# Performance work log

Measured on AMD Instinct MI355X. Metric: run time of the kernel, lower is better.

The kernel has to match this reference:

```python
import jax, jax.numpy as jnp
import numpy as np

MODEL_DIM = 1024
NUM_HEADS = 16
HEAD_DIM = MODEL_DIM // NUM_HEADS  # 64
MAX_SEQ = 1024
MAX_REL = 8


def setup_inputs() -> dict:
    key = jax.random.key(0)
    ks = jax.random.split(key, 5)
    B, S = 4, 1024
    x = jax.random.normal(ks[0], (B, S, MODEL_DIM), jnp.float32)
    W_in = jax.random.normal(ks[1], (MODEL_DIM, MODEL_DIM), jnp.float32) * 0.02
    W_out = jax.random.normal(ks[2], (MODEL_DIM, MODEL_DIM), jnp.float32) * 0.02
    # learned synthesized attention scores [1, H, max_seq, max_seq]
    attn_scores = jax.random.normal(ks[3], (1, NUM_HEADS, MAX_SEQ, MAX_SEQ), jnp.float32) * 0.05
    # relative-position VALUE embedding table [2*max_rel+1, head_dim]
    rel_values = jax.random.normal(ks[4], (2 * MAX_REL + 1, HEAD_DIM), jnp.float32) * 0.02
    return {"x": x, "W_in": W_in, "W_out": W_out,
            "attn_scores": attn_scores, "rel_values": rel_values}


def reference(x, W_in, W_out, attn_scores, rel_values):
    B, S, D = x.shape
    H, hd = NUM_HEADS, HEAD_DIM
    # in-projection (no bias), split heads: [B, H, S, hd]
    value = (x @ W_in.T).reshape(B, S, H, hd).transpose(0, 2, 1, 3)
    # learned (random-synthesizer) scores, sliced to seq len, broadcast over batch
    scores = attn_scores[:, :, :S, :S]              # [1, H, S, S]
    probs = jax.nn.softmax(scores, axis=-1)          # [1, H, S, S]
    probs = jnp.broadcast_to(probs, (B, H, S, S))
    # attention output: probs @ V
    out = jnp.einsum('bhsj,bhjd->bhsd', probs, value)  # [B, H, S, hd]
    # relative-position value contribution
    r = jnp.arange(S)
    dist = r[None, :] - r[:, None]                   # [S, S]
    idx = jnp.clip(dist, -MAX_REL, MAX_REL) + MAX_REL
    rel_emb = rel_values[idx]                        # [S, S, hd]
    out = out + jnp.einsum('bhsj,sjd->bhsd', probs, rel_emb)
    # join heads and out-project
    out = out.transpose(0, 2, 1, 3).reshape(B, S, H * hd)
    return out @ W_out.T                             # [B, S, D]
```

## Files before the change

kernel.cpp:

```cpp
#include <hip/hip_runtime.h>

typedef unsigned short ushort_t;
typedef __attribute__((ext_vector_type(4))) short short4_t;
typedef __attribute__((ext_vector_type(8))) short short8;
typedef __attribute__((ext_vector_type(4))) float floatx4;
typedef __attribute__((ext_vector_type(8))) __bf16 bf16x8;

__device__ __forceinline__ ushort_t f2b(float f) {
  union { float f; unsigned int i; } t; t.f = f;
  unsigned int u = t.i;
  return (ushort_t)((u + 0x7fffu + ((u >> 16) & 1u)) >> 16);
}

__device__ __forceinline__ floatx4 mfma16(short8 a, short8 b, floatx4 c) {
  return __builtin_amdgcn_mfma_f32_16x16x32_bf16(
      __builtin_bit_cast(bf16x8, a), __builtin_bit_cast(bf16x8, b), c, 0, 0, 0);
}

__device__ __forceinline__ void gload16(const void* g, void* l) {
  __builtin_amdgcn_global_load_lds(
      (const __attribute__((address_space(1))) void*)g,
      (__attribute__((address_space(3))) void*)l, 16, 0, 0);
}

__global__ __launch_bounds__(256) void k_f2b_all(
    const float* __restrict__ x, const float* __restrict__ Wi,
    const float* __restrict__ Wo, ushort_t* __restrict__ xb,
    ushort_t* __restrict__ Wib, ushort_t* __restrict__ Wob)
{
  const float* in; ushort_t* out; int i;
  if (blockIdx.x < 2048)      { in = x;  out = xb;  i = (blockIdx.x * 256 + threadIdx.x) * 8; }
  else if (blockIdx.x < 2560) { in = Wi; out = Wib; i = ((blockIdx.x - 2048) * 256 + threadIdx.x) * 8; }
  else                        { in = Wo; out = Wob; i = ((blockIdx.x - 2560) * 256 + threadIdx.x) * 8; }
  float4 a = *reinterpret_cast<const float4*>(in + i);
  float4 b = *reinterpret_cast<const float4*>(in + i + 4);
  short8 o;
  o[0] = (short)f2b(a.x); o[1] = (short)f2b(a.y);
  o[2] = (short)f2b(a.z); o[3] = (short)f2b(a.w);
  o[4] = (short)f2b(b.x); o[5] = (short)f2b(b.y);
  o[6] = (short)f2b(b.z); o[7] = (short)f2b(b.w);
  *reinterpret_cast<short8*>(out + i) = o;
}

#define STG(kt, buf, SLOTSZ)                                                \
  {                                                                         \
    const int k0 = (kt) << 6;                                               \
    _Pragma("unroll")                                                       \
    for (int cc = 0; cc < 2; ++cc) {                                        \
      int c = threadIdx.x + (cc << 9);                                      \
      int r = c >> 3, cb = c & 7;                                           \
      int sc = k0 + ((cb ^ (r & 7)) << 3);                                  \
      gload16(A0 + (size_t)r * 1024 + sc, (char*)sA + (buf) * SLOTSZ + c * 16); \
      gload16(B0 + (size_t)r * 1024 + sc, (char*)sB + (buf) * SLOTSZ + c * 16); \
    }                                                                       \
  }

#define KSTEP_COMPUTE(bA, bB)                                               \
  _Pragma("unroll")                                                         \
  for (int kk = 0; kk < 2; ++kk) {                                          \
    const int cs = (kk << 2) + lk;                                          \
    short8 af[4], bf[2];                                                    \
    _Pragma("unroll")                                                       \
    for (int i = 0; i < 4; ++i) {                                           \
      int ra = (wm << 6) + (i << 4) + l15;                                  \
      af[i] = *reinterpret_cast<const short8*>(                             \
          (bA) + ra * 128 + ((cs ^ (ra & 7)) << 4));                        \
    }                                                                       \
    _Pragma("unroll")                                                       \
    for (int j = 0; j < 2; ++j) {                                           \
      int rb = (wn << 5) + (j << 4) + l15;                                  \
      bf[j] = *reinterpret_cast<const short8*>(                             \
          (bB) + rb * 128 + ((cs ^ (rb & 7)) << 4));                        \
    }                                                                       \
    __builtin_amdgcn_s_setprio(1);                                          \
    _Pragma("unroll")                                                       \
    for (int i = 0; i < 4; ++i)                                             \
      _Pragma("unroll")                                                     \
      for (int j = 0; j < 2; ++j)                                           \
        acc[i][j] = mfma16(af[i], bf[j], acc[i][j]);                        \
    __builtin_amdgcn_s_setprio(0);                                          \
  }

__device__ __forceinline__ void gemm128_loop4(
    const ushort_t* __restrict__ A0, const ushort_t* __restrict__ B0,
    ushort_t* sA, ushort_t* sB, floatx4 (&acc)[4][2])
{
  const int lane = threadIdx.x & 63, wave = threadIdx.x >> 6;
  const int wm = wave & 1, wn = wave >> 1;
  const int l15 = lane & 15, lk = lane >> 4;

  STG(0, 0, 16384);
  STG(1, 1, 16384);
  for (int kt = 0; kt < 16; ++kt) {
    if (kt < 14) {
      STG(kt + 2, (kt + 2) & 3, 16384);
      asm volatile("s_waitcnt vmcnt(8)" ::: "memory");
    } else if (kt == 14) {
      asm volatile("s_waitcnt vmcnt(4)" ::: "memory");
    } else {
      asm volatile("s_waitcnt vmcnt(0)" ::: "memory");
    }
    __builtin_amdgcn_s_barrier();
    const char* bA = (const char*)sA + (kt & 3) * 16384;
    const char* bB = (const char*)sB + (kt & 3) * 16384;
    KSTEP_COMPUTE(bA, bB);
  }
}

__device__ __forceinline__ void gemm128_loop2(
    const ushort_t* __restrict__ A0, const ushort_t* __restrict__ B0,
    ushort_t* sA, ushort_t* sB, floatx4 (&acc)[4][2])
{
  const int lane = threadIdx.x & 63, wave = threadIdx.x >> 6;
  const int wm = wave & 1, wn = wave >> 1;
  const int l15 = lane & 15, lk = lane >> 4;

  STG(0, 0, 16384);
  for (int kt = 0; kt < 16; ++kt) {
    __syncthreads();
    if (kt < 15) STG(kt + 1, (kt + 1) & 1, 16384);
    const char* bA = (const char*)sA + (kt & 1) * 16384;
    const char* bB = (const char*)sB + (kt & 1) * 16384;
    KSTEP_COMPUTE(bA, bB);
  }
}

__device__ __forceinline__ int xcd_swz(int bid) {
  return ((bid & 7) << 5) | (bid >> 3);
}

__global__ __launch_bounds__(512) void k_fused_sm_xw(
    const float* __restrict__ S, const float* __restrict__ relv,
    ushort_t* __restrict__ P, float* __restrict__ R,
    const ushort_t* __restrict__ W, const ushort_t* __restrict__ X,
    ushort_t* __restrict__ Yt)
{
  __shared__ __align__(16) char smem[65536];

  if (blockIdx.x < 256) {
    ushort_t* sA = (ushort_t*)smem;
    ushort_t* sB = (ushort_t*)(smem + 32768);
    const int lg = xcd_swz(blockIdx.x);
    const int m0 = (lg & 7) << 7, n0 = (lg >> 3) << 7;
    const ushort_t* A0 = W + (size_t)m0 * 1024;
    const ushort_t* B0 = X + (size_t)n0 * 1024;
    floatx4 acc[4][2] = {};
    gemm128_loop2(A0, B0, sA, sB, acc);

    const int lane = threadIdx.x & 63, wave = threadIdx.x >> 6;
    const int wm = wave & 1, wn = wave >> 1;
    const int l15 = lane & 15, lk = lane >> 4;
#pragma unroll
    for (int i = 0; i < 4; ++i)
#pragma unroll
      for (int j = 0; j < 2; ++j)
#pragma unroll
        for (int rr = 0; rr < 4; ++rr) {
          int wrow = m0 + (wm << 6) + (i << 4) + (lk << 2) + rr;
          int col  = n0 + (wn << 5) + (j << 4) + l15;
          int h = wrow >> 6, d = wrow & 63;
          int b = col >> 10, s = col & 1023;
          Yt[(((size_t)((h << 2) + b) << 6) + d) * 1024 + s] = f2b(acc[i][j][rr]);
        }
    return;
  }

  float (*mid)[16] = (float (*)[16])smem;
  const int wave = threadIdx.x >> 6, lane = threadIdx.x & 63;
  const int row = (blockIdx.x - 256) * 8 + wave;
  const int s = row & 1023;
  const float* src = S + (size_t)row * 1024;

  float v[4][4];
#pragma unroll
  for (int c = 0; c < 4; ++c) {
    float4 raw = *reinterpret_cast<const float4*>(src + c * 256 + lane * 4);
    v[c][0] = raw.x; v[c][1] = raw.y; v[c][2] = raw.z; v[c][3] = raw.w;
  }
  float m = -1e30f;
#pragma unroll
  for (int c = 0; c < 4; ++c)
#pragma unroll
    for (int e = 0; e < 4; ++e) m = fmaxf(m, v[c][e]);
#pragma unroll
  for (int d = 32; d; d >>= 1) m = fmaxf(m, __shfl_xor(m, d));

  float p[4][4];
  float tot = 0.f, sA = 0.f, sB = 0.f;
#pragma unroll
  for (int c = 0; c < 4; ++c) {
#pragma unroll
    for (int e = 0; e < 4; ++e) {
      int j = c * 256 + lane * 4 + e;
      float pe = __expf(v[c][e] - m);
      p[c][e] = pe;
      tot += pe;
      sA += (j <= s - 8) ? pe : 0.f;
      sB += (j >= s + 8) ? pe : 0.f;
    }
  }
#pragma unroll
  for (int d = 32; d; d >>= 1) {
    tot += __shfl_xor(tot, d);
    sA  += __shfl_xor(sA, d);
    sB  += __shfl_xor(sB, d);
  }
  const float inv = 1.0f / tot;

  if (lane < 16) mid[wave][lane] = 0.f;
  __syncthreads();
#pragma unroll
  for (int c = 0; c < 4; ++c) {
#pragma unroll
    for (int e = 0; e < 4; ++e) {
      int j = c * 256 + lane * 4 + e;
      int tt = j - (s - 7);
      if (tt >= 0 && tt < 15) mid[wave][tt] = p[c][e];
    }
  }
  __syncthreads();

  float acc = sA * relv[lane] + sB * relv[16 * 64 + lane];
#pragma unroll
  for (int tt = 0; tt < 15; ++tt)
    acc += mid[wave][tt] * relv[(1 + tt) * 64 + lane];
  R[(size_t)row * 64 + lane] = acc * inv;

#pragma unroll
  for (int c = 0; c < 4; ++c) {
    short4_t o;
#pragma unroll
    for (int e = 0; e < 4; ++e) o[e] = (short)f2b(p[c][e] * inv);
    *reinterpret_cast<short4_t*>(P + (size_t)row * 1024 + c * 256 + lane * 4) = o;
  }
}

__global__ __launch_bounds__(512) void k_head_pv(
    const ushort_t* __restrict__ P, const ushort_t* __restrict__ Yt,
    const float* __restrict__ R, ushort_t* __restrict__ O)
{
  __shared__ ushort_t sA[4 * 128 * 64];
  __shared__ ushort_t sB[4 * 128 * 64];
  const int lg = xcd_swz(blockIdx.x);
  const int h = lg >> 4, rem = lg & 15;
  const int m0 = (rem >> 1) << 7, n0 = (rem & 1) << 7;
  floatx4 acc[4][2] = {};
  gemm128_loop4(P + ((size_t)h << 20) + (size_t)m0 * 1024,
                Yt + ((size_t)h << 18) + (size_t)n0 * 1024, sA, sB, acc);

  const int lane = threadIdx.x & 63, wave = threadIdx.x >> 6;
  const int wm = wave & 1, wn = wave >> 1;
  const int l15 = lane & 15, lk = lane >> 4;
#pragma unroll
  for (int i = 0; i < 4; ++i)
#pragma unroll
    for (int j = 0; j < 2; ++j)
#pragma unroll
      for (int rr = 0; rr < 4; ++rr) {
        int sr = m0 + (wm << 6) + (i << 4) + (lk << 2) + rr;
        int c  = n0 + (wn << 5) + (j << 4) + l15;
        int b = c >> 6, d = c & 63;
        float val = acc[i][j][rr] + R[(((size_t)h << 10) + sr) * 64 + d];
        O[((size_t)b << 20) + ((size_t)sr << 10) + (h << 6) + d] = f2b(val);
      }
}

__global__ __launch_bounds__(512) void k_gemm_out(
    const ushort_t* __restrict__ A, const ushort_t* __restrict__ B,
    float* __restrict__ C)
{
  __shared__ ushort_t sA[4 * 128 * 64];
  __shared__ ushort_t sB[4 * 128 * 64];
  const int lg = xcd_swz(blockIdx.x);
  const int m0 = (lg >> 3) << 7, n0 = (lg & 7) << 7;
  floatx4 acc[4][2] = {};
  gemm128_loop4(A + (size_t)m0 * 1024, B + (size_t)n0 * 1024, sA, sB, acc);

  const int lane = threadIdx.x & 63, wave = threadIdx.x >> 6;
  const int wm = wave & 1, wn = wave >> 1;
  const int l15 = lane & 15, lk = lane >> 4;
#pragma unroll
  for (int i = 0; i < 4; ++i)
#pragma unroll
    for (int j = 0; j < 2; ++j)
#pragma unroll
      for (int rr = 0; rr < 4; ++rr) {
        int rowg = m0 + (wm << 6) + (i << 4) + (lk << 2) + rr;
        int colg = n0 + (wn << 5) + (j << 4) + l15;
        C[(size_t)rowg * 1024 + colg] = acc[i][j][rr];
      }
}

extern "C" void kernel_launch(void* const* d_in, const int* in_sizes, int n_in,
                              void* d_out, int out_size, void* d_ws, size_t ws_size,
                              hipStream_t stream)
{
  const float* x     = (const float*)d_in[0];
  const float* W_in  = (const float*)d_in[1];
  const float* W_out = (const float*)d_in[2];
  const float* attn  = (const float*)d_in[3];
  const float* relv  = (const float*)d_in[4];
  float* out = (float*)d_out;

  char* ws = (char*)d_ws;
  ushort_t* xb  = (ushort_t*)(ws);
  ushort_t* Wib = (ushort_t*)(ws + (8u << 20));
  ushort_t* Wob = (ushort_t*)(ws + (10u << 20));
  ushort_t* P   = (ushort_t*)(ws + (12u << 20));
  float*    R   = (float*)   (ws + (44u << 20));
  ushort_t* Yt  = (ushort_t*)(ws + (48u << 20));
  ushort_t* O   = (ushort_t*)(ws + (56u << 20));

  k_f2b_all<<<3072, 256, 0, stream>>>(x, W_in, W_out, xb, Wib, Wob);
  k_fused_sm_xw<<<2304, 512, 0, stream>>>(attn, relv, P, R, Wib, xb, Yt);
  k_head_pv<<<256, 512, 0, stream>>>(P, Yt, R, O);
  k_gemm_out<<<256, 512, 0, stream>>>(O, Wob, out);
}
```

Before: 65.43 us.

## Regroup softmax with f32-to-bf16 conversion; run x·W_in GEMM as standalone 4-stage kernel

Moves the per-row softmax and relative-value reduction out of the kernel shared with the input-projection GEMM and into the conversion kernel, using 256-thread blocks with 4 rows each. The input-projection GEMM becomes its own kernel using the deeper 4-buffer pipelined loop instead of the 2-buffer one. The aim is to stop the large softmax grid and the GEMM blocks competing inside one launch, and to use the better-pipelined GEMM. The trade-off is the same number of launches with different grouping, and the GEMM can no longer overlap with softmax work.

```diff
diff --git a/kernel.cpp b/kernel.cpp
--- a/kernel.cpp
+++ b/kernel.cpp
@@ -23,26 +23,101 @@
       (__attribute__((address_space(3))) void*)l, 16, 0, 0);
 }
 
-__global__ __launch_bounds__(256) void k_f2b_all(
+__global__ __launch_bounds__(256) void k_sm_f2b(
+    const float* __restrict__ S, const float* __restrict__ relv,
+    ushort_t* __restrict__ P, float* __restrict__ R,
     const float* __restrict__ x, const float* __restrict__ Wi,
     const float* __restrict__ Wo, ushort_t* __restrict__ xb,
     ushort_t* __restrict__ Wib, ushort_t* __restrict__ Wob)
 {
-  const float* in; ushort_t* out; int i;
-  if (blockIdx.x < 2048)      { in = x;  out = xb;  i = (blockIdx.x * 256 + threadIdx.x) * 8; }
-  else if (blockIdx.x < 2560) { in = Wi; out = Wib; i = ((blockIdx.x - 2048) * 256 + threadIdx.x) * 8; }
-  else                        { in = Wo; out = Wob; i = ((blockIdx.x - 2560) * 256 + threadIdx.x) * 8; }
-  float4 a = *reinterpret_cast<const float4*>(in + i);
-  float4 b = *reinterpret_cast<const float4*>(in + i + 4);
-  short8 o;
-  o[0] = (short)f2b(a.x); o[1] = (short)f2b(a.y);
-  o[2] = (short)f2b(a.z); o[3] = (short)f2b(a.w);
-  o[4] = (short)f2b(b.x); o[5] = (short)f2b(b.y);
-  o[6] = (short)f2b(b.z); o[7] = (short)f2b(b.w);
-  *reinterpret_cast<short8*>(out + i) = o;
-}
-
-#define STG(kt, buf, SLOTSZ)                                                \
+  __shared__ float mid[4][16];
+
+  if (blockIdx.x < 3072) {
+    const float* in; ushort_t* out; int i;
+    if (blockIdx.x < 2048)      { in = x;  out = xb;  i = (blockIdx.x * 256 + threadIdx.x) * 8; }
+    else if (blockIdx.x < 2560) { in = Wi; out = Wib; i = ((blockIdx.x - 2048) * 256 + threadIdx.x) * 8; }
+    else                        { in = Wo; out = Wob; i = ((blockIdx.x - 2560) * 256 + threadIdx.x) * 8; }
+    float4 a = *reinterpret_cast<const float4*>(in + i);
+    float4 b = *reinterpret_cast<const float4*>(in + i + 4);
+    short8 o;
+    o[0] = (short)f2b(a.x); o[1] = (short)f2b(a.y);
+    o[2] = (short)f2b(a.z); o[3] = (short)f2b(a.w);
+    o[4] = (short)f2b(b.x); o[5] = (short)f2b(b.y);
+    o[6] = (short)f2b(b.z); o[7] = (short)f2b(b.w);
+    *reinterpret_cast<short8*>(out + i) = o;
+    return;
+  }
+
+  const int wave = threadIdx.x >> 6, lane = threadIdx.x & 63;
+  const int row = (blockIdx.x - 3072) * 4 + wave;
+  const int s = row & 1023;
+  const float* src = S + (size_t)row * 1024;
+
+  float v[4][4];
+#pragma unroll
+  for (int c = 0; c < 4; ++c) {
+    float4 raw = *reinterpret_cast<const float4*>(src + c * 256 + lane * 4);
+    v[c][0] = raw.x; v[c][1] = raw.y; v[c][2] = raw.z; v[c][3] = raw.w;
+  }
+  float m = -1e30f;
+#pragma unroll
+  for (int c = 0; c < 4; ++c)
+#pragma unroll
+    for (int e = 0; e < 4; ++e) m = fmaxf(m, v[c][e]);
+#pragma unroll
+  for (int d = 32; d; d >>= 1) m = fmaxf(m, __shfl_xor(m, d));
+
+  float p[4][4];
+  float tot = 0.f, sA = 0.f, sB = 0.f;
+#pragma unroll
+  for (int c = 0; c < 4; ++c) {
+#pragma unroll
+    for (int e = 0; e < 4; ++e) {
+      int j = c * 256 + lane * 4 + e;
+      float pe = __expf(v[c][e] - m);
+      p[c][e] = pe;
+      tot += pe;
+      sA += (j <= s - 8) ? pe : 0.f;
+      sB += (j >= s + 8) ? pe : 0.f;
+    }
+  }
+#pragma unroll
+  for (int d = 32; d; d >>= 1) {
+    tot += __shfl_xor(tot, d);
+    sA  += __shfl_xor(sA, d);
+    sB  += __shfl_xor(sB, d);
+  }
+  const float inv = 1.0f / tot;
+
+  if (lane < 16) mid[wave][lane] = 0.f;
+  __syncthreads();
+#pragma unroll
+  for (int c = 0; c < 4; ++c) {
+#pragma unroll
+    for (int e = 0; e < 4; ++e) {
+      int j = c * 256 + lane * 4 + e;
+      int tt = j - (s - 7);
+      if (tt >= 0 && tt < 15) mid[wave][tt] = p[c][e];
+    }
+  }
+  __syncthreads();
+
+  float acc = sA * relv[lane] + sB * relv[16 * 64 + lane];
+#pragma unroll
+  for (int tt = 0; tt < 15; ++tt)
+    acc += mid[wave][tt] * relv[(1 + tt) * 64 + lane];
+  R[(size_t)row * 64 + lane] = acc * inv;
+
+#pragma unroll
+  for (int c = 0; c < 4; ++c) {
+    short4_t o;
+#pragma unroll
+    for (int e = 0; e < 4; ++e) o[e] = (short)f2b(p[c][e] * inv);
+    *reinterpret_cast<short4_t*>(P + (size_t)row * 1024 + c * 256 + lane * 4) = o;
+  }
+}
+
+#define STG(kt, buf)                                                        \
   {                                                                         \
     const int k0 = (kt) << 6;                                               \
     _Pragma("unroll")                                                       \
@@ -50,8 +125,8 @@
       int c = threadIdx.x + (cc << 9);                                      \
       int r = c >> 3, cb = c & 7;                                           \
       int sc = k0 + ((cb ^ (r & 7)) << 3);                                  \
-      gload16(A0 + (size_t)r * 1024 + sc, (char*)sA + (buf) * SLOTSZ + c * 16); \
-      gload16(B0 + (size_t)r * 1024 + sc, (char*)sB + (buf) * SLOTSZ + c * 16); \
+      gload16(A0 + (size_t)r * 1024 + sc, (char*)sA + (buf) * 16384 + c * 16); \
+      gload16(B0 + (size_t)r * 1024 + sc, (char*)sB + (buf) * 16384 + c * 16); \
     }                                                                       \
   }
 
@@ -89,11 +164,11 @@
   const int wm = wave & 1, wn = wave >> 1;
   const int l15 = lane & 15, lk = lane >> 4;
 
-  STG(0, 0, 16384);
-  STG(1, 1, 16384);
+  STG(0, 0);
+  STG(1, 1);
   for (int kt = 0; kt < 16; ++kt) {
     if (kt < 14) {
-      STG(kt + 2, (kt + 2) & 3, 16384);
+      STG(kt + 2, (kt + 2) & 3);
       asm volatile("s_waitcnt vmcnt(8)" ::: "memory");
     } else if (kt == 14) {
       asm volatile("s_waitcnt vmcnt(4)" ::: "memory");
@@ -107,132 +182,38 @@
   }
 }
 
-__device__ __forceinline__ void gemm128_loop2(
-    const ushort_t* __restrict__ A0, const ushort_t* __restrict__ B0,
-    ushort_t* sA, ushort_t* sB, floatx4 (&acc)[4][2])
-{
+__device__ __forceinline__ int xcd_swz(int bid) {
+  return ((bid & 7) << 5) | (bid >> 3);
+}
+
+__global__ __launch_bounds__(512) void k_gemm_xw(
+    const ushort_t* __restrict__ W, const ushort_t* __restrict__ X,
+    ushort_t* __restrict__ Yt)
+{
+  __shared__ ushort_t sA[4 * 128 * 64];
+  __shared__ ushort_t sB[4 * 128 * 64];
+  const int lg = xcd_swz(blockIdx.x);
+  const int m0 = (lg & 7) << 7, n0 = (lg >> 3) << 7;
+  const ushort_t* A0 = W + (size_t)m0 * 1024;
+  const ushort_t* B0 = X + (size_t)n0 * 1024;
+  floatx4 acc[4][2] = {};
+  gemm128_loop4(A0, B0, sA, sB, acc);
+
   const int lane = threadIdx.x & 63, wave = threadIdx.x >> 6;
   const int wm = wave & 1, wn = wave >> 1;
   const int l15 = lane & 15, lk = lane >> 4;
-
-  STG(0, 0, 16384);
-  for (int kt = 0; kt < 16; ++kt) {
-    __syncthreads();
-    if (kt < 15) STG(kt + 1, (kt + 1) & 1, 16384);
-    const char* bA = (const char*)sA + (kt & 1) * 16384;
-    const char* bB = (const char*)sB + (kt & 1) * 16384;
-    KSTEP_COMPUTE(bA, bB);
-  }
-}
-
-__device__ __forceinline__ int xcd_swz(int bid) {
-  return ((bid & 7) << 5) | (bid >> 3);
-}
-
-__global__ __launch_bounds__(512) void k_fused_sm_xw(
-    const float* __restrict__ S, const float* __restrict__ relv,
-    ushort_t* __restrict__ P, float* __restrict__ R,
-    const ushort_t* __restrict__ W, const ushort_t* __restrict__ X,
-    ushort_t* __restrict__ Yt)
-{
-  __shared__ __align__(16) char smem[65536];
-
-  if (blockIdx.x < 256) {
-    ushort_t* sA = (ushort_t*)smem;
-    ushort_t* sB = (ushort_t*)(smem + 32768);
-    const int lg = xcd_swz(blockIdx.x);
-    const int m0 = (lg & 7) << 7, n0 = (lg >> 3) << 7;
-    const ushort_t* A0 = W + (size_t)m0 * 1024;
-    const ushort_t* B0 = X + (size_t)n0 * 1024;
-    floatx4 acc[4][2] = {};
-    gemm128_loop2(A0, B0, sA, sB, acc);
-
-    const int lane = threadIdx.x & 63, wave = threadIdx.x >> 6;
-    const int wm = wave & 1, wn = wave >> 1;
-    const int l15 = lane & 15, lk = lane >> 4;
-#pragma unroll
-    for (int i = 0; i < 4; ++i)
-#pragma unroll
-      for (int j = 0; j < 2; ++j)
-#pragma unroll
-        for (int rr = 0; rr < 4; ++rr) {
-          int wrow = m0 + (wm << 6) + (i << 4) + (lk << 2) + rr;
-          int col  = n0 + (wn << 5) + (j << 4) + l15;
-          int h = wrow >> 6, d = wrow & 63;
-          int b = col >> 10, s = col & 1023;
-          Yt[(((size_t)((h << 2) + b) << 6) + d) * 1024 + s] = f2b(acc[i][j][rr]);
-        }
-    return;
-  }
-
-  float (*mid)[16] = (float (*)[16])smem;
-  const int wave = threadIdx.x >> 6, lane = threadIdx.x & 63;
-  const int row = (blockIdx.x - 256) * 8 + wave;
-  const int s = row & 1023;
-  const float* src = S + (size_t)row * 1024;
-
-  float v[4][4];
-#pragma unroll
-  for (int c = 0; c < 4; ++c) {
-    float4 raw = *reinterpret_cast<const float4*>(src + c * 256 + lane * 4);
-    v[c][0] = raw.x; v[c][1] = raw.y; v[c][2] = raw.z; v[c][3] = raw.w;
-  }
-  float m = -1e30f;
-#pragma unroll
-  for (int c = 0; c < 4; ++c)
-#pragma unroll
-    for (int e = 0; e < 4; ++e) m = fmaxf(m, v[c][e]);
-#pragma unroll
-  for (int d = 32; d; d >>= 1) m = fmaxf(m, __shfl_xor(m, d));
-
-  float p[4][4];
-  float tot = 0.f, sA = 0.f, sB = 0.f;
-#pragma unroll
-  for (int c = 0; c < 4; ++c) {
-#pragma unroll
-    for (int e = 0; e < 4; ++e) {
-      int j = c * 256 + lane * 4 + e;
-      float pe = __expf(v[c][e] - m);
-      p[c][e] = pe;
-      tot += pe;
-      sA += (j <= s - 8) ? pe : 0.f;
-      sB += (j >= s + 8) ? pe : 0.f;
-    }
-  }
-#pragma unroll
-  for (int d = 32; d; d >>= 1) {
-    tot += __shfl_xor(tot, d);
-    sA  += __shfl_xor(sA, d);
-    sB  += __shfl_xor(sB, d);
-  }
-  const float inv = 1.0f / tot;
-
-  if (lane < 16) mid[wave][lane] = 0.f;
-  __syncthreads();
-#pragma unroll
-  for (int c = 0; c < 4; ++c) {
-#pragma unroll
-    for (int e = 0; e < 4; ++e) {
-      int j = c * 256 + lane * 4 + e;
-      int tt = j - (s - 7);
-      if (tt >= 0 && tt < 15) mid[wave][tt] = p[c][e];
-    }
-  }
-  __syncthreads();
-
-  float acc = sA * relv[lane] + sB * relv[16 * 64 + lane];
-#pragma unroll
-  for (int tt = 0; tt < 15; ++tt)
-    acc += mid[wave][tt] * relv[(1 + tt) * 64 + lane];
-  R[(size_t)row * 64 + lane] = acc * inv;
-
-#pragma unroll
-  for (int c = 0; c < 4; ++c) {
-    short4_t o;
-#pragma unroll
-    for (int e = 0; e < 4; ++e) o[e] = (short)f2b(p[c][e] * inv);
-    *reinterpret_cast<short4_t*>(P + (size_t)row * 1024 + c * 256 + lane * 4) = o;
-  }
+#pragma unroll
+  for (int i = 0; i < 4; ++i)
+#pragma unroll
+    for (int j = 0; j < 2; ++j)
+#pragma unroll
+      for (int rr = 0; rr < 4; ++rr) {
+        int wrow = m0 + (wm << 6) + (i << 4) + (lk << 2) + rr;
+        int col  = n0 + (wn << 5) + (j << 4) + l15;
+        int h = wrow >> 6, d = wrow & 63;
+        int b = col >> 10, s = col & 1023;
+        Yt[(((size_t)((h << 2) + b) << 6) + d) * 1024 + s] = f2b(acc[i][j][rr]);
+      }
 }
 
 __global__ __launch_bounds__(512) void k_head_pv(
@@ -244,9 +225,10 @@
   const int lg = xcd_swz(blockIdx.x);
   const int h = lg >> 4, rem = lg & 15;
   const int m0 = (rem >> 1) << 7, n0 = (rem & 1) << 7;
+  const ushort_t* A0 = P + ((size_t)h << 20) + (size_t)m0 * 1024;
+  const ushort_t* B0 = Yt + ((size_t)h << 18) + (size_t)n0 * 1024;
   floatx4 acc[4][2] = {};
-  gemm128_loop4(P + ((size_t)h << 20) + (size_t)m0 * 1024,
-                Yt + ((size_t)h << 18) + (size_t)n0 * 1024, sA, sB, acc);
+  gemm128_loop4(A0, B0, sA, sB, acc);
 
   const int lane = threadIdx.x & 63, wave = threadIdx.x >> 6;
   const int wm = wave & 1, wn = wave >> 1;
@@ -273,8 +255,10 @@
   __shared__ ushort_t sB[4 * 128 * 64];
   const int lg = xcd_swz(blockIdx.x);
   const int m0 = (lg >> 3) << 7, n0 = (lg & 7) << 7;
+  const ushort_t* A0 = A + (size_t)m0 * 1024;
+  const ushort_t* B0 = B + (size_t)n0 * 1024;
   floatx4 acc[4][2] = {};
-  gemm128_loop4(A + (size_t)m0 * 1024, B + (size_t)n0 * 1024, sA, sB, acc);
+  gemm128_loop4(A0, B0, sA, sB, acc);
 
   const int lane = threadIdx.x & 63, wave = threadIdx.x >> 6;
   const int wm = wave & 1, wn = wave >> 1;
@@ -311,8 +295,8 @@
   ushort_t* Yt  = (ushort_t*)(ws + (48u << 20));
   ushort_t* O   = (ushort_t*)(ws + (56u << 20));
 
-  k_f2b_all<<<3072, 256, 0, stream>>>(x, W_in, W_out, xb, Wib, Wob);
-  k_fused_sm_xw<<<2304, 512, 0, stream>>>(attn, relv, P, R, Wib, xb, Yt);
+  k_sm_f2b<<<7168, 256, 0, stream>>>(attn, relv, P, R, x, W_in, W_out, xb, Wib, Wob);
+  k_gemm_xw<<<256, 512, 0, stream>>>(Wib, xb, Yt);
   k_head_pv<<<256, 512, 0, stream>>>(P, Yt, R, O);
   k_gemm_out<<<256, 512, 0, stream>>>(O, Wob, out);
 }
```

Result: no change. 64.97 us (-0.7%).
